# Optimization experiments

Hardware: AMD Instinct MI355X
Metric: run time of the kernel (lower is better)

Reference implementation:

```python
import jax, jax.numpy as jnp
import numpy as np

N = 20000
M = 32          # max_neighbors
IN_DIM = 256
OUT_DIM = 256
H = 4           # num_heads
D = OUT_DIM // H  # head_dim = 64
LN_EPS = 1e-5
NEG_INF = -1.0e9


def setup_inputs() -> dict:
    key = jax.random.key(0)
    ks = jax.random.split(key, 6)
    h = jax.random.normal(ks[0], (N, IN_DIM), dtype=jnp.float32)
    neighbor_idx = jax.random.randint(ks[1], (N, M), 0, N, dtype=jnp.int32)
    neighbor_mask = jax.random.randint(ks[2], (N, M), 0, 2, dtype=jnp.int32)
    # parameters (xavier-ish scaling)
    W = jax.random.normal(ks[3], (IN_DIM, OUT_DIM), dtype=jnp.float32) / np.sqrt(IN_DIM)
    a_l = jax.random.normal(ks[4], (H, D), dtype=jnp.float32) / np.sqrt(D)
    a_r = jax.random.normal(ks[5], (H, D), dtype=jnp.float32) / np.sqrt(D)
    ln_gamma = jnp.ones((OUT_DIM,), dtype=jnp.float32)
    ln_beta = jnp.zeros((OUT_DIM,), dtype=jnp.float32)
    return {"h": h, "neighbor_idx": neighbor_idx, "neighbor_mask": neighbor_mask,
            "W": W, "a_l": a_l, "a_r": a_r, "ln_gamma": ln_gamma, "ln_beta": ln_beta}


def reference(h, neighbor_idx, neighbor_mask, W, a_l, a_r, ln_gamma, ln_beta):
    h_proj = h @ W                                   # [N, OUT_DIM]
    h_heads = h_proj.reshape(N, H, D)                # [N, H, D]
    # per-node score halves; gathering scalars instead of full features for er
    el = jnp.einsum('nhd,hd->nh', h_heads, a_l)      # [N, H]
    er_node = jnp.einsum('nhd,hd->nh', h_heads, a_r) # [N, H]
    er = er_node[neighbor_idx]                       # [N, M, H]
    e = jax.nn.leaky_relu(el[:, None, :] + er, negative_slope=0.2)  # [N, M, H]
    e = jnp.where(neighbor_mask[:, :, None] == 0, NEG_INF, e)
    alpha = jax.nn.softmax(e, axis=1)                # softmax over neighbors
    neigh_h = h_heads[neighbor_idx]                  # [N, M, H, D]
    out_heads = jnp.einsum('nmh,nmhd->nhd', alpha, neigh_h)
    H_cat = out_heads.reshape(N, OUT_DIM)
    res = h_proj                                     # in_dim == out_dim -> res_proj is None
    out = jax.nn.gelu(H_cat + res, approximate=False)
    # LayerNorm over last dim
    mu = jnp.mean(out, axis=-1, keepdims=True)
    var = jnp.var(out, axis=-1, keepdims=True)
    out = (out - mu) * jax.lax.rsqrt(var + LN_EPS) * ln_gamma + ln_beta
    return out
```

## Files before the change

kernel.cpp:

```cpp
#include <hip/hip_runtime.h>
#include <math.h>

#define N_NODES 20000
#define M_NEI   32
#define DIM     256
#define H_HEADS 4
#define D_HEAD  64
#define LN_EPS  1e-5f
#define NEG_INF -1.0e9f
#define APAD    264

using short8  = __attribute__((ext_vector_type(8))) short;
using short4v = __attribute__((ext_vector_type(4))) short;
using floatx4 = __attribute__((ext_vector_type(4))) float;

__device__ __forceinline__ float bf2f(unsigned short u) {
    union { unsigned int i; float f; } c; c.i = ((unsigned int)u) << 16; return c.f;
}
__device__ __forceinline__ unsigned short f2bf(float f) {
    union { float f; unsigned int i; } c; c.f = f;
    unsigned int x = c.i;
    x += 0x7fffu + ((x >> 16) & 1u);
    return (unsigned short)(x >> 16);
}
__device__ __forceinline__ bool in_is_fp32(const void* gamma) {
    return *(const unsigned int*)gamma == 0x3F800000u;
}

__global__ void k_transpose(const void* __restrict__ W, const void* __restrict__ gamma,
                            unsigned short* __restrict__ Wt) {
    const bool f32 = in_is_fp32(gamma);
    int n = blockIdx.x;
    int k = threadIdx.x;
    float w = f32 ? ((const float*)W)[(size_t)k * DIM + n]
                  : bf2f(((const unsigned short*)W)[(size_t)k * DIM + n]);
    Wt[(size_t)n * DIM + k] = f2bf(w);
}

__global__ __launch_bounds__(512) void k_gemm(const void* __restrict__ A,
                                              const void* __restrict__ gamma,
                                              const unsigned short* __restrict__ Bt,
                                              const void* __restrict__ al,
                                              const void* __restrict__ ar,
                                              unsigned short* __restrict__ hp_h,
                                              float* __restrict__ el_h,
                                              float* __restrict__ er_h) {
    __shared__ unsigned short sA[64][APAD];
    const bool f32 = in_is_fp32(gamma);
    const int t    = threadIdx.x;
    const int wave = t >> 6;
    const int lane = t & 63;
    const int m0   = blockIdx.x * 64;

    #pragma unroll
    for (int it = 0; it < 4; ++it) {
        int chunk = it * 512 + t;
        int row   = chunk >> 5;
        int c16   = chunk & 31;
        int grow  = m0 + row;
        short8 v = {};
        if (grow < N_NODES) {
            if (!f32) {
                v = *(const short8*)((const unsigned short*)A + (size_t)grow * DIM + c16 * 8);
            } else {
                const float* ap = (const float*)A + (size_t)grow * DIM + c16 * 8;
                #pragma unroll
                for (int j = 0; j < 8; ++j) v[j] = (short)f2bf(ap[j]);
            }
        }
        *(short8*)&sA[row][c16 * 8] = v;
    }
    __syncthreads();

    const int r    = lane & 15;
    const int quad = lane >> 4;
    const int hd   = wave & 3;
    const int rh   = wave >> 2;
    const int n0   = hd * 64;

    floatx4 acc[2][4];
    #pragma unroll
    for (int rf = 0; rf < 2; ++rf)
        #pragma unroll
        for (int c = 0; c < 4; ++c) acc[rf][c] = (floatx4){0.f, 0.f, 0.f, 0.f};

    #pragma unroll
    for (int k0 = 0; k0 < DIM; k0 += 32) {
        short8 a0 = *(const short8*)&sA[rh * 32 + r][k0 + quad * 8];
        short8 a1 = *(const short8*)&sA[rh * 32 + 16 + r][k0 + quad * 8];
        #pragma unroll
        for (int c = 0; c < 4; ++c) {
            short8 b = *(const short8*)(Bt + (size_t)(n0 + c * 16 + r) * DIM + k0 + quad * 8);
            acc[0][c] = __builtin_amdgcn_mfma_f32_16x16x32_bf16(a0, b, acc[0][c], 0, 0, 0);
            acc[1][c] = __builtin_amdgcn_mfma_f32_16x16x32_bf16(a1, b, acc[1][c], 0, 0, 0);
        }
    }

    float alv[4], arv[4];
    #pragma unroll
    for (int c = 0; c < 4; ++c) {
        int col = n0 + c * 16 + r;
        if (f32) { alv[c] = ((const float*)al)[col]; arv[c] = ((const float*)ar)[col]; }
        else     { alv[c] = bf2f(((const unsigned short*)al)[col]);
                   arv[c] = bf2f(((const unsigned short*)ar)[col]); }
    }

    #pragma unroll
    for (int rf = 0; rf < 2; ++rf) {
        #pragma unroll
        for (int rr = 0; rr < 4; ++rr) {
            int row = m0 + rh * 32 + rf * 16 + quad * 4 + rr;
            float sl = 0.f, sr = 0.f;
            #pragma unroll
            for (int c = 0; c < 4; ++c) {
                float v = acc[rf][c][rr];
                sl += v * alv[c];
                sr += v * arv[c];
                if (row < N_NODES)
                    hp_h[((size_t)hd * N_NODES + row) * D_HEAD + c * 16 + r] = f2bf(v);
            }
            #pragma unroll
            for (int off = 1; off < 16; off <<= 1) {
                sl += __shfl_xor(sl, off);
                sr += __shfl_xor(sr, off);
            }
            if (r == 0 && row < N_NODES) {
                el_h[(size_t)hd * N_NODES + row] = sl;
                er_h[(size_t)hd * N_NODES + row] = sr;
            }
        }
    }
}

__global__ __launch_bounds__(256) void k_attn_h(const int* __restrict__ nidx,
                                                const int* __restrict__ nmask,
                                                const unsigned short* __restrict__ hp_h,
                                                const float* __restrict__ el_h,
                                                const float* __restrict__ er_h,
                                                unsigned short* __restrict__ out_h) {
    const int wave = threadIdx.x >> 6;
    const int lane = threadIdx.x & 63;
    const int hd   = blockIdx.x & 3;
    const int n    = (blockIdx.x >> 2) * 4 + wave;

    const int m   = lane & 31;
    const int idx = nidx[(size_t)n * M_NEI + m];
    const int msk = nmask[(size_t)n * M_NEI + m];

    const float elv = el_h[(size_t)hd * N_NODES + n];
    const float erv = er_h[(size_t)hd * N_NODES + idx];
    float e = elv + erv;
    e = (e > 0.f) ? e : 0.2f * e;
    e = msk ? e : NEG_INF;

    float mx = e;
    #pragma unroll
    for (int off = 1; off < 32; off <<= 1) mx = fmaxf(mx, __shfl_xor(mx, off, 32));
    float a = expf(e - mx);
    float sm = a;
    #pragma unroll
    for (int off = 1; off < 32; off <<= 1) sm += __shfl_xor(sm, off, 32);
    a /= sm;

    const int g = lane >> 3;
    const int s = lane & 7;
    const unsigned short* tbl = hp_h + (size_t)hd * N_NODES * D_HEAD + s * 8;

    float acc[8];
    #pragma unroll
    for (int i = 0; i < 8; ++i) acc[i] = 0.f;

    #pragma unroll
    for (int it = 0; it < 4; ++it) {
        const int mm   = it * 8 + g;
        const int rowi = __shfl(idx, mm);
        const float aa = __shfl(a, mm);
        short8 v = *(const short8*)(tbl + (size_t)rowi * D_HEAD);
        #pragma unroll
        for (int i = 0; i < 8; ++i) acc[i] += aa * bf2f((unsigned short)v[i]);
    }
    #pragma unroll
    for (int off = 8; off < 64; off <<= 1)
        #pragma unroll
        for (int i = 0; i < 8; ++i) acc[i] += __shfl_xor(acc[i], off);

    if (g == 0) {
        short8 o;
        #pragma unroll
        for (int i = 0; i < 8; ++i) o[i] = (short)f2bf(acc[i]);
        *(short8*)(out_h + ((size_t)hd * N_NODES + n) * D_HEAD + s * 8) = o;
    }
}

__global__ __launch_bounds__(256) void k_final(const unsigned short* __restrict__ hp_h,
                                               const unsigned short* __restrict__ out_h,
                                               const void* __restrict__ gamma,
                                               const void* __restrict__ beta,
                                               void* __restrict__ out) {
    const bool f32 = in_is_fp32(gamma);
    const int wave = threadIdx.x >> 6;
    const int lane = threadIdx.x & 63;
    const int n    = blockIdx.x * 4 + wave;
    const int h    = lane >> 4;
    const int d0   = (lane & 15) * 4;

    const size_t off = ((size_t)h * N_NODES + n) * D_HEAD + d0;
    short4v hv = *(const short4v*)(hp_h + off);
    short4v ov = *(const short4v*)(out_h + off);

    float x[4], s1 = 0.f, s2 = 0.f;
    #pragma unroll
    for (int i = 0; i < 4; ++i) {
        float xi = bf2f((unsigned short)ov[i]) + bf2f((unsigned short)hv[i]);
        xi = 0.5f * xi * (1.f + erff(xi * 0.70710678118654752f));
        x[i] = xi;
        s1 += xi;
        s2 += xi * xi;
    }
    #pragma unroll
    for (int offv = 1; offv < 64; offv <<= 1) {
        s1 += __shfl_xor(s1, offv);
        s2 += __shfl_xor(s2, offv);
    }
    const float mu  = s1 * (1.f / 256.f);
    float var = s2 * (1.f / 256.f) - mu * mu;
    var = fmaxf(var, 0.f);
    const float inv = rsqrtf(var + LN_EPS);

    if (f32) {
        const float* gp = (const float*)gamma + lane * 4;
        const float* bp = (const float*)beta  + lane * 4;
        float* op = (float*)out + (size_t)n * DIM + lane * 4;
        #pragma unroll
        for (int i = 0; i < 4; ++i)
            op[i] = (x[i] - mu) * inv * gp[i] + bp[i];
    } else {
        const unsigned short* gp = (const unsigned short*)gamma + lane * 4;
        const unsigned short* bp = (const unsigned short*)beta  + lane * 4;
        short4v o;
        #pragma unroll
        for (int i = 0; i < 4; ++i) {
            float y = (x[i] - mu) * inv * bf2f(gp[i]) + bf2f(bp[i]);
            o[i] = (short)f2bf(y);
        }
        *(short4v*)((unsigned short*)out + (size_t)n * DIM + lane * 4) = o;
    }
}

extern "C" void kernel_launch(void* const* d_in, const int* in_sizes, int n_in,
                              void* d_out, int out_size, void* d_ws, size_t ws_size,
                              hipStream_t stream) {
    const void* h     = d_in[0];
    const int*  nidx  = (const int*)d_in[1];
    const int*  nmask = (const int*)d_in[2];
    const void* W     = d_in[3];
    const void* al    = d_in[4];
    const void* ar    = d_in[5];
    const void* gamma = d_in[6];
    const void* beta  = d_in[7];

    unsigned short* Wt    = (unsigned short*)d_ws;
    unsigned short* hp_h  = (unsigned short*)((char*)d_ws + 131072);
    unsigned short* out_h = (unsigned short*)((char*)d_ws + 10371072);
    float* el_h = (float*)((char*)d_ws + 20611072);
    float* er_h = (float*)((char*)d_ws + 20931072);

    k_transpose<<<DIM, DIM, 0, stream>>>(W, gamma, Wt);
    k_gemm<<<(N_NODES + 63) / 64, 512, 0, stream>>>(h, gamma, Wt, al, ar, hp_h, el_h, er_h);
    k_attn_h<<<N_NODES, 256, 0, stream>>>(nidx, nmask, hp_h, el_h, er_h, out_h);
    k_final<<<N_NODES / 4, 256, 0, stream>>>(hp_h, out_h, gamma, beta, d_out);
}
```

Baseline: 150.8 us.

## Restructure attention to one thread-group per node with LDS-staged softmax weights

```diff
diff --git a/kernel.cpp b/kernel.cpp
--- a/kernel.cpp
+++ b/kernel.cpp
@@ -13,9 +13,15 @@
 using short8  = __attribute__((ext_vector_type(8))) short;
 using short4v = __attribute__((ext_vector_type(4))) short;
 using floatx4 = __attribute__((ext_vector_type(4))) float;
+using floatx2 = __attribute__((ext_vector_type(2))) float;
+using uintx4  = __attribute__((ext_vector_type(4))) unsigned int;
+using intx4   = __attribute__((ext_vector_type(4))) int;
 
 __device__ __forceinline__ float bf2f(unsigned short u) {
     union { unsigned int i; float f; } c; c.i = ((unsigned int)u) << 16; return c.f;
+}
+__device__ __forceinline__ float u2f(unsigned int i) {
+    union { unsigned int i; float f; } c; c.i = i; return c.f;
 }
 __device__ __forceinline__ unsigned short f2bf(float f) {
     union { float f; unsigned int i; } c; c.f = f;
@@ -37,7 +43,7 @@
     Wt[(size_t)n * DIM + k] = f2bf(w);
 }
 
-__global__ __launch_bounds__(512) void k_gemm(const void* __restrict__ A,
+__global__ __launch_bounds__(256) void k_gemm(const void* __restrict__ A,
                                               const void* __restrict__ gamma,
                                               const unsigned short* __restrict__ Bt,
                                               const void* __restrict__ al,
@@ -45,54 +51,45 @@
                                               unsigned short* __restrict__ hp_h,
                                               float* __restrict__ el_h,
                                               float* __restrict__ er_h) {
-    __shared__ unsigned short sA[64][APAD];
+    __shared__ unsigned short sA[16][APAD];
     const bool f32 = in_is_fp32(gamma);
     const int t    = threadIdx.x;
-    const int wave = t >> 6;
-    const int lane = t & 63;
-    const int m0   = blockIdx.x * 64;
-
-    #pragma unroll
-    for (int it = 0; it < 4; ++it) {
-        int chunk = it * 512 + t;
+    const int m0   = blockIdx.x * 16;
+
+    #pragma unroll
+    for (int it = 0; it < 2; ++it) {
+        int chunk = it * 256 + t;
         int row   = chunk >> 5;
         int c16   = chunk & 31;
-        int grow  = m0 + row;
-        short8 v = {};
-        if (grow < N_NODES) {
-            if (!f32) {
-                v = *(const short8*)((const unsigned short*)A + (size_t)grow * DIM + c16 * 8);
-            } else {
-                const float* ap = (const float*)A + (size_t)grow * DIM + c16 * 8;
-                #pragma unroll
-                for (int j = 0; j < 8; ++j) v[j] = (short)f2bf(ap[j]);
-            }
+        short8 v;
+        if (!f32) {
+            v = *(const short8*)((const unsigned short*)A + (size_t)(m0 + row) * DIM + c16 * 8);
+        } else {
+            const float* ap = (const float*)A + (size_t)(m0 + row) * DIM + c16 * 8;
+            #pragma unroll
+            for (int j = 0; j < 8; ++j) v[j] = (short)f2bf(ap[j]);
         }
         *(short8*)&sA[row][c16 * 8] = v;
     }
     __syncthreads();
 
+    const int hd   = t >> 6;
+    const int lane = t & 63;
     const int r    = lane & 15;
     const int quad = lane >> 4;
-    const int hd   = wave & 3;
-    const int rh   = wave >> 2;
     const int n0   = hd * 64;
 
-    floatx4 acc[2][4];
-    #pragma unroll
-    for (int rf = 0; rf < 2; ++rf)
-        #pragma unroll
-        for (int c = 0; c < 4; ++c) acc[rf][c] = (floatx4){0.f, 0.f, 0.f, 0.f};
+    floatx4 acc[4];
+    #pragma unroll
+    for (int c = 0; c < 4; ++c) acc[c] = (floatx4){0.f, 0.f, 0.f, 0.f};
 
     #pragma unroll
     for (int k0 = 0; k0 < DIM; k0 += 32) {
-        short8 a0 = *(const short8*)&sA[rh * 32 + r][k0 + quad * 8];
-        short8 a1 = *(const short8*)&sA[rh * 32 + 16 + r][k0 + quad * 8];
+        short8 a = *(const short8*)&sA[r][k0 + quad * 8];
         #pragma unroll
         for (int c = 0; c < 4; ++c) {
             short8 b = *(const short8*)(Bt + (size_t)(n0 + c * 16 + r) * DIM + k0 + quad * 8);
-            acc[0][c] = __builtin_amdgcn_mfma_f32_16x16x32_bf16(a0, b, acc[0][c], 0, 0, 0);
-            acc[1][c] = __builtin_amdgcn_mfma_f32_16x16x32_bf16(a1, b, acc[1][c], 0, 0, 0);
+            acc[c] = __builtin_amdgcn_mfma_f32_16x16x32_bf16(a, b, acc[c], 0, 0, 0);
         }
     }
 
@@ -106,28 +103,24 @@
     }
 
     #pragma unroll
-    for (int rf = 0; rf < 2; ++rf) {
-        #pragma unroll
-        for (int rr = 0; rr < 4; ++rr) {
-            int row = m0 + rh * 32 + rf * 16 + quad * 4 + rr;
-            float sl = 0.f, sr = 0.f;
-            #pragma unroll
-            for (int c = 0; c < 4; ++c) {
-                float v = acc[rf][c][rr];
-                sl += v * alv[c];
-                sr += v * arv[c];
-                if (row < N_NODES)
-                    hp_h[((size_t)hd * N_NODES + row) * D_HEAD + c * 16 + r] = f2bf(v);
-            }
-            #pragma unroll
-            for (int off = 1; off < 16; off <<= 1) {
-                sl += __shfl_xor(sl, off);
-                sr += __shfl_xor(sr, off);
-            }
-            if (r == 0 && row < N_NODES) {
-                el_h[(size_t)hd * N_NODES + row] = sl;
-                er_h[(size_t)hd * N_NODES + row] = sr;
-            }
+    for (int rr = 0; rr < 4; ++rr) {
+        const int row = m0 + quad * 4 + rr;
+        float sl = 0.f, sr = 0.f;
+        #pragma unroll
+        for (int c = 0; c < 4; ++c) {
+            float v = acc[c][rr];
+            sl += v * alv[c];
+            sr += v * arv[c];
+            hp_h[((size_t)hd * N_NODES + row) * D_HEAD + c * 16 + r] = f2bf(v);
+        }
+        #pragma unroll
+        for (int off = 1; off < 16; off <<= 1) {
+            sl += __shfl_xor(sl, off);
+            sr += __shfl_xor(sr, off);
+        }
+        if (r == 0) {
+            el_h[(size_t)hd * N_NODES + row] = sl;
+            er_h[(size_t)hd * N_NODES + row] = sr;
         }
     }
 }
@@ -138,58 +131,69 @@
                                                 const float* __restrict__ el_h,
                                                 const float* __restrict__ er_h,
                                                 unsigned short* __restrict__ out_h) {
-    const int wave = threadIdx.x >> 6;
-    const int lane = threadIdx.x & 63;
-    const int hd   = blockIdx.x & 3;
-    const int n    = (blockIdx.x >> 2) * 4 + wave;
-
-    const int m   = lane & 31;
-    const int idx = nidx[(size_t)n * M_NEI + m];
-    const int msk = nmask[(size_t)n * M_NEI + m];
-
-    const float elv = el_h[(size_t)hd * N_NODES + n];
-    const float erv = er_h[(size_t)hd * N_NODES + idx];
-    float e = elv + erv;
-    e = (e > 0.f) ? e : 0.2f * e;
-    e = msk ? e : NEG_INF;
-
-    float mx = e;
-    #pragma unroll
-    for (int off = 1; off < 32; off <<= 1) mx = fmaxf(mx, __shfl_xor(mx, off, 32));
-    float a = expf(e - mx);
-    float sm = a;
-    #pragma unroll
-    for (int off = 1; off < 32; off <<= 1) sm += __shfl_xor(sm, off, 32);
-    a /= sm;
-
-    const int g = lane >> 3;
-    const int s = lane & 7;
+    __shared__ int   s_idx[32][33];
+    __shared__ float s_al[32][33];
+
+    const int hd  = blockIdx.x & 3;
+    const int nb0 = (blockIdx.x >> 2) * 32;
+    const int t   = threadIdx.x;
+
+    {
+        const int m   = t & 31;
+        const int sub = t >> 5;
+        #pragma unroll
+        for (int it = 0; it < 4; ++it) {
+            const int nl  = it * 8 + sub;
+            const int n   = nb0 + nl;
+            const int idx = nidx[(size_t)n * M_NEI + m];
+            const int msk = nmask[(size_t)n * M_NEI + m];
+            float e = el_h[(size_t)hd * N_NODES + n] + er_h[(size_t)hd * N_NODES + idx];
+            e = (e > 0.f) ? e : 0.2f * e;
+            e = msk ? e : NEG_INF;
+            float mx = e;
+            #pragma unroll
+            for (int off = 1; off < 32; off <<= 1) mx = fmaxf(mx, __shfl_xor(mx, off, 32));
+            float a = expf(e - mx);
+            float sm = a;
+            #pragma unroll
+            for (int off = 1; off < 32; off <<= 1) sm += __shfl_xor(sm, off, 32);
+            s_idx[nl][m] = idx;
+            s_al[nl][m]  = a / sm;
+        }
+    }
+    __syncthreads();
+
+    const int wave = t >> 6;
+    const int lane = t & 63;
+    const int g    = lane >> 3;
+    const int s    = lane & 7;
+    const int nl   = wave * 8 + g;
+    const int n    = nb0 + nl;
     const unsigned short* tbl = hp_h + (size_t)hd * N_NODES * D_HEAD + s * 8;
 
-    float acc[8];
-    #pragma unroll
-    for (int i = 0; i < 8; ++i) acc[i] = 0.f;
-
-    #pragma unroll
-    for (int it = 0; it < 4; ++it) {
-        const int mm   = it * 8 + g;
-        const int rowi = __shfl(idx, mm);
-        const float aa = __shfl(a, mm);
-        short8 v = *(const short8*)(tbl + (size_t)rowi * D_HEAD);
-        #pragma unroll
-        for (int i = 0; i < 8; ++i) acc[i] += aa * bf2f((unsigned short)v[i]);
-    }
-    #pragma unroll
-    for (int off = 8; off < 64; off <<= 1)
-        #pragma unroll
-        for (int i = 0; i < 8; ++i) acc[i] += __shfl_xor(acc[i], off);
-
-    if (g == 0) {
-        short8 o;
-        #pragma unroll
-        for (int i = 0; i < 8; ++i) o[i] = (short)f2bf(acc[i]);
-        *(short8*)(out_h + ((size_t)hd * N_NODES + n) * D_HEAD + s * 8) = o;
-    }
+    floatx2 acc[4];
+    #pragma unroll
+    for (int j = 0; j < 4; ++j) acc[j] = (floatx2){0.f, 0.f};
+
+    #pragma unroll
+    for (int m = 0; m < M_NEI; ++m) {
+        const int   rowi = s_idx[nl][m];
+        const float aa   = s_al[nl][m];
+        uintx4 u = *(const uintx4*)(tbl + (size_t)rowi * D_HEAD);
+        #pragma unroll
+        for (int j = 0; j < 4; ++j) {
+            floatx2 f = { u2f(u[j] << 16), u2f(u[j] & 0xffff0000u) };
+            acc[j] += (floatx2){aa, aa} * f;
+        }
+    }
+
+    short8 o;
+    #pragma unroll
+    for (int j = 0; j < 4; ++j) {
+        o[2 * j]     = (short)f2bf(acc[j][0]);
+        o[2 * j + 1] = (short)f2bf(acc[j][1]);
+    }
+    *(short8*)(out_h + ((size_t)hd * N_NODES + n) * D_HEAD + s * 8) = o;
 }
 
 __global__ __launch_bounds__(256) void k_final(const unsigned short* __restrict__ hp_h,
@@ -266,7 +270,7 @@
     float* er_h = (float*)((char*)d_ws + 20931072);
 
     k_transpose<<<DIM, DIM, 0, stream>>>(W, gamma, Wt);
-    k_gemm<<<(N_NODES + 63) / 64, 512, 0, stream>>>(h, gamma, Wt, al, ar, hp_h, el_h, er_h);
-    k_attn_h<<<N_NODES, 256, 0, stream>>>(nidx, nmask, hp_h, el_h, er_h, out_h);
+    k_gemm<<<N_NODES / 16, 256, 0, stream>>>(h, gamma, Wt, al, ar, hp_h, el_h, er_h);
+    k_attn_h<<<H_HEADS * (N_NODES / 32), 256, 0, stream>>>(nidx, nmask, hp_h, el_h, er_h, out_h);
     k_final<<<N_NODES / 4, 256, 0, stream>>>(hp_h, out_h, gamma, beta, d_out);
 }
```

Measured after the change: 141.4 us. 6.2% less time.
